# Optimization experiments

Hardware: AMD Instinct MI355X
Metric: run time of the kernel (lower is better)

Reference implementation:

```python
import jax, jax.numpy as jnp
import numpy as np

B, CI, CO, H, W, E, R, K = 32, 128, 256, 64, 64, 8, 16, 3


def setup_inputs() -> dict:
    key = jax.random.key(0)
    ks = jax.random.split(key, 12)
    def n(k, shape, scale):
        return jax.random.normal(k, shape, dtype=jnp.float32) * scale
    return {
        "x": n(ks[0], (B, CI, H, W), 1.0),
        "experts": n(ks[1], (E, CO, CI, K, K), 0.1),
        # routing SE: C -> C/R -> C -> E (1x1 convs == dense on pooled vec)
        "rw1": n(ks[2], (CI // R, CI), 0.05), "rb1": jnp.zeros((CI // R,), jnp.float32),
        "rw2": n(ks[3], (CI, CI // R), 0.05), "rb2": jnp.zeros((CI,), jnp.float32),
        "rw3": n(ks[4], (E, CI), 0.05),      "rb3": jnp.zeros((E,), jnp.float32),
        # channel attention SE on output: CO -> CO/R -> CO
        "aw1": n(ks[5], (CO // R, CO), 0.05), "ab1": jnp.zeros((CO // R,), jnp.float32),
        "aw2": n(ks[6], (CO, CO // R), 0.05), "ab2": jnp.zeros((CO,), jnp.float32),
    }


def reference(x, experts, rw1, rb1, rw2, rb2, rw3, rb3, aw1, ab1, aw2, ab2):
    # --- routing: SE-style gate -> softmax over experts ---
    pooled = x.mean(axis=(2, 3))                       # [B, CI]
    h = jax.nn.relu(pooled @ rw1.T + rb1)              # [B, CI/R]
    s = jax.nn.sigmoid(h @ rw2.T + rb2)                # [B, CI]
    rweights = jax.nn.softmax(s @ rw3.T + rb3, axis=1) # [B, E]
    # --- per-sample expert kernel combination ---
    w = jnp.einsum('be,eoihw->boihw', rweights, experts)  # [B, CO, CI, K, K]
    # --- per-sample conv (== grouped conv with groups=B) via vmap ---
    def conv1(xi, wi):
        # xi: [CI,H,W], wi: [CO,CI,K,K]
        return jax.lax.conv_general_dilated(
            xi[None], wi, window_strides=(1, 1), padding=[(1, 1), (1, 1)],
            dimension_numbers=('NCHW', 'OIHW', 'NCHW'))[0]
    out = jax.vmap(conv1)(x, w)                        # [B, CO, H, W]
    # --- channel attention on output ---
    p = out.mean(axis=(2, 3))                          # [B, CO]
    ca = jax.nn.sigmoid(jax.nn.relu(p @ aw1.T + ab1) @ aw2.T + ab2)
    return out * ca[:, :, None, None]
```

## Files before the change

### kernel.cpp

```cpp
#include <hip/hip_runtime.h>
#include <hip/hip_bf16.h>


#define BB 32
#define CI_ 128
#define CO_ 256
#define HW_ 4096
#define KK 1152

typedef unsigned short u16;
typedef __attribute__((ext_vector_type(8))) __bf16 bf16x8;
typedef __attribute__((ext_vector_type(4))) float floatx4;

typedef const __attribute__((address_space(1))) void* gptr_t;
typedef __attribute__((address_space(3))) void* sptr_t;

__device__ __forceinline__ void gload_lds16(const void* g, void* s) {
  __builtin_amdgcn_global_load_lds((gptr_t)g, (sptr_t)s, 16, 0, 0);
}

__global__ __launch_bounds__(256) void k_stats(const float* __restrict__ x,
                                               float* __restrict__ Sr,
                                               float* __restrict__ pooled,
                                               unsigned* __restrict__ zp) {
  int blk = blockIdx.x;
  if (blk == 0 && threadIdx.x < 64) zp[threadIdx.x] = 0u;
  int b = blk >> 7, ci = blk & 127;
  const float4* xp = (const float4*)(x + ((size_t)(b * CI_ + ci) << 12));
  float T = 0.f, r0 = 0.f, r63 = 0.f, c0 = 0.f, c63 = 0.f;
  __shared__ float corn[4];
  __shared__ float wsum[4][5];
  int tid = threadIdx.x;
  for (int k = 0; k < 4; k++) {
    int i4 = tid + (k << 8);
    float4 v = xp[i4];
    float vv[4] = {v.x, v.y, v.z, v.w};
#pragma unroll
    for (int c = 0; c < 4; c++) {
      int e = (i4 << 2) + c;
      int y = e >> 6, xx = e & 63;
      float val = vv[c];
      T += val;
      if (y == 0) r0 += val;
      if (y == 63) r63 += val;
      if (xx == 0) c0 += val;
      if (xx == 63) c63 += val;
      if (e == 0)    corn[0] = val;
      if (e == 63)   corn[1] = val;
      if (e == 4032) corn[2] = val;
      if (e == 4095) corn[3] = val;
    }
  }
  for (int off = 32; off; off >>= 1) {
    T   += __shfl_down(T, off);
    r0  += __shfl_down(r0, off);
    r63 += __shfl_down(r63, off);
    c0  += __shfl_down(c0, off);
    c63 += __shfl_down(c63, off);
  }
  int w = tid >> 6, lane = tid & 63;
  if (lane == 0) { wsum[w][0]=T; wsum[w][1]=r0; wsum[w][2]=r63; wsum[w][3]=c0; wsum[w][4]=c63; }
  __syncthreads();
  if (tid == 0) {
    T   = wsum[0][0]+wsum[1][0]+wsum[2][0]+wsum[3][0];
    r0  = wsum[0][1]+wsum[1][1]+wsum[2][1]+wsum[3][1];
    r63 = wsum[0][2]+wsum[1][2]+wsum[2][2]+wsum[3][2];
    c0  = wsum[0][3]+wsum[1][3]+wsum[2][3]+wsum[3][3];
    c63 = wsum[0][4]+wsum[1][4]+wsum[2][4]+wsum[3][4];
    pooled[b * CI_ + ci] = T * (1.0f / 4096.0f);
#pragma unroll
    for (int ky = 0; ky < 3; ky++) {
#pragma unroll
      for (int kx = 0; kx < 3; kx++) {
        int dy = ky - 1, dx = kx - 1;
        float s = T;
        if (dy == -1) s -= r63;
        if (dy ==  1) s -= r0;
        if (dx == -1) s -= c63;
        if (dx ==  1) s -= c0;
        if (dy != 0 && dx != 0) s += corn[(dy == -1 ? 2 : 0) + (dx == -1 ? 1 : 0)];
        Sr[(b * 9 + ky * 3 + kx) * CI_ + ci] = s * (1.0f / 4096.0f);
      }
    }
  }
}

__global__ __launch_bounds__(256) void k_transpose(const float* __restrict__ x,
                                                   u16* __restrict__ xt) {
  int blk = blockIdx.x;
  int b = blk >> 6, y = blk & 63;
  __shared__ u16 ts[64][130];
  int tid = threadIdx.x;
  const float* xb = x + ((size_t)b << 19) + (y << 6);
  for (int k = 0; k < 32; k++) {
    int i = tid + (k << 8);
    int ci = i >> 6, xx = i & 63;
    float v = xb[(size_t)ci * 4096 + xx];
    __hip_bfloat16 h = __float2bfloat16(v);
    ts[xx][ci] = *(const u16*)&h;
  }
  __syncthreads();
  uint2* ot = (uint2*)(xt + ((size_t)b * HW_ + y * 64) * CI_);
  for (int k = 0; k < 8; k++) {
    int j = tid + (k << 8);
    int pix = j >> 5, cq = (j & 31) << 2;
    uint2 val;
    u16* pv = (u16*)&val;
    pv[0] = ts[pix][cq]; pv[1] = ts[pix][cq + 1];
    pv[2] = ts[pix][cq + 2]; pv[3] = ts[pix][cq + 3];
    ot[j] = val;
  }
}

__global__ __launch_bounds__(128) void k_route(const float* __restrict__ pooled,
    const float* __restrict__ rw1, const float* __restrict__ rb1,
    const float* __restrict__ rw2, const float* __restrict__ rb2,
    const float* __restrict__ rw3, const float* __restrict__ rb3,
    float* __restrict__ r) {
  int b = blockIdx.x, tid = threadIdx.x;
  __shared__ float ps[128], hs[8], ss[128], lg[8];
  ps[tid] = pooled[b * 128 + tid];
  __syncthreads();
  if (tid < 8) {
    float a = rb1[tid];
    for (int c = 0; c < 128; c++) a += ps[c] * rw1[tid * 128 + c];
    hs[tid] = fmaxf(a, 0.f);
  }
  __syncthreads();
  {
    float a = rb2[tid];
    for (int j = 0; j < 8; j++) a += hs[j] * rw2[tid * 8 + j];
    ss[tid] = 1.f / (1.f + expf(-a));
  }
  __syncthreads();
  if (tid < 8) {
    float a = rb3[tid];
    for (int c = 0; c < 128; c++) a += ss[c] * rw3[tid * 128 + c];
    lg[tid] = a;
  }
  __syncthreads();
  if (tid == 0) {
    float m = lg[0];
    for (int e = 1; e < 8; e++) m = fmaxf(m, lg[e]);
    float s = 0.f, ex[8];
    for (int e = 0; e < 8; e++) { ex[e] = expf(lg[e] - m); s += ex[e]; }
    for (int e = 0; e < 8; e++) r[b * 8 + e] = ex[e] / s;
  }
}

__global__ __launch_bounds__(128) void k_combine(const float* __restrict__ experts,
                                                 const float* __restrict__ r,
                                                 __hip_bfloat16* __restrict__ wr) {
  int blk = blockIdx.x;
  int co = blk >> 5, b = blk & 31;
  int ci = threadIdx.x;
  __shared__ float rs[8];
  if (ci < 8) rs[ci] = r[b * 8 + ci];
  __syncthreads();
  float acc[9] = {0.f, 0.f, 0.f, 0.f, 0.f, 0.f, 0.f, 0.f, 0.f};
  for (int e = 0; e < 8; e++) {
    const float* ep = experts + (((size_t)e * 256 + co) * 128 + ci) * 9;
    float wv = rs[e];
#pragma unroll
    for (int k = 0; k < 9; k++) acc[k] += wv * ep[k];
  }
  __hip_bfloat16* wrow = wr + (size_t)(b * 256 + co) * KK;
#pragma unroll
  for (int k = 0; k < 9; k++) wrow[k * 128 + ci] = __float2bfloat16(acc[k]);
}

__global__ __launch_bounds__(64) void k_pout(const __hip_bfloat16* __restrict__ wr,
                                             const float* __restrict__ Sr,
                                             float* __restrict__ p) {
  int blk = blockIdx.x;
  int b = blk >> 8, co = blk & 255;
  int t = threadIdx.x;
  const __hip_bfloat16* wrow = wr + (size_t)(b * 256 + co) * KK;
  const float* sb = Sr + b * KK;
  float a = 0.f;
  for (int i = t; i < KK; i += 64) a += __bfloat162float(wrow[i]) * sb[i];
  for (int off = 32; off; off >>= 1) a += __shfl_down(a, off);
  if (t == 0) p[b * 256 + co] = a;
}

__global__ __launch_bounds__(256) void k_catt(const float* __restrict__ p,
    const float* __restrict__ aw1, const float* __restrict__ ab1,
    const float* __restrict__ aw2, const float* __restrict__ ab2,
    float* __restrict__ ca) {
  int b = blockIdx.x, tid = threadIdx.x;
  __shared__ float ps[256], ts[16];
  ps[tid] = p[b * 256 + tid];
  __syncthreads();
  if (tid < 16) {
    float a = ab1[tid];
    for (int c = 0; c < 256; c++) a += ps[c] * aw1[tid * 256 + c];
    ts[tid] = fmaxf(a, 0.f);
  }
  __syncthreads();
  float a = ab2[tid];
  for (int j = 0; j < 16; j++) a += ts[j] * aw2[tid * 16 + j];
  ca[b * 256 + tid] = 1.f / (1.f + expf(-a));
}

__global__ __launch_bounds__(256) void k_conv(const u16* __restrict__ xt,
                                              const u16* __restrict__ wr,
                                              const float* __restrict__ ca,
                                              const u16* __restrict__ zp,
                                              float* __restrict__ out) {
  int blk = blockIdx.x;
  int rp = blk & 31, coT = (blk >> 5) & 1, b = blk >> 6;
  int y0 = rp * 2;
  int coBase = coT * 128;
  int tid = threadIdx.x;
  int w = tid >> 6, lane = tid & 63;
  int wm = w & 1, wn = w >> 1;
  int quad = lane >> 4, l15 = lane & 15;
  int cl = lane & 3;

  __shared__ __align__(16) u16 As[128 * 32];
  __shared__ __align__(16) u16 Bs[128 * 32];

  const u16* aSrc[2];
  int dstOff[2], chB[2], ylocB[2], xlocB[2];
#pragma unroll
  for (int inst = 0; inst < 2; inst++) {
    int rr = w * 32 + inst * 16 + (lane >> 2);
    int s = (rr ^ (rr >> 2)) & 3;
    int ch = cl ^ s;
    aSrc[inst] = wr + (size_t)(b * 256 + coBase + rr) * KK + ch * 8;
    dstOff[inst] = (w * 32 + inst * 16) * 32 + lane * 8;
    chB[inst] = ch;
    ylocB[inst] = rr >> 6;
    xlocB[inst] = rr & 63;
  }

  int aOff[4], bOff[4];
#pragma unroll
  for (int i = 0; i < 4; i++) {
    int m = wm * 64 + i * 16 + l15;
    aOff[i] = m * 32 + ((quad ^ ((m ^ (m >> 2)) & 3)) << 3);
    int n = wn * 64 + i * 16 + l15;
    bOff[i] = n * 32 + ((quad ^ ((n ^ (n >> 2)) & 3)) << 3);
  }

  floatx4 acc[4][4];
#pragma unroll
  for (int i = 0; i < 4; i++)
#pragma unroll
    for (int j = 0; j < 4; j++) acc[i][j] = floatx4{0.f, 0.f, 0.f, 0.f};

  for (int kidx = 0; kidx < 9; kidx++) {
    int ky = kidx / 3, kx = kidx - ky * 3;
    const u16* bSrc[2];
#pragma unroll
    for (int inst = 0; inst < 2; inst++) {
      int ys = y0 + ylocB[inst] + ky - 1;
      int xs = xlocB[inst] + kx - 1;
      bool valid = ((unsigned)ys < 64u) && ((unsigned)xs < 64u);
      bSrc[inst] = valid ? (xt + ((size_t)(b * HW_ + ys * 64 + xs) << 7) + chB[inst] * 8)
                         : (zp + chB[inst] * 8);
    }
    const u16* aS0 = aSrc[0] + kidx * 128;
    const u16* aS1 = aSrc[1] + kidx * 128;
#pragma unroll
    for (int cib = 0; cib < 4; cib++) {
      __syncthreads();
      gload_lds16(aS0 + cib * 32, &As[dstOff[0]]);
      gload_lds16(aS1 + cib * 32, &As[dstOff[1]]);
      gload_lds16(bSrc[0] + cib * 32, &Bs[dstOff[0]]);
      gload_lds16(bSrc[1] + cib * 32, &Bs[dstOff[1]]);
      __syncthreads();
      bf16x8 af[4], bfv[4];
#pragma unroll
      for (int i = 0; i < 4; i++) af[i] = *(const bf16x8*)&As[aOff[i]];
#pragma unroll
      for (int j = 0; j < 4; j++) bfv[j] = *(const bf16x8*)&Bs[bOff[j]];
#pragma unroll
      for (int i = 0; i < 4; i++)
#pragma unroll
        for (int j = 0; j < 4; j++)
          acc[i][j] = __builtin_amdgcn_mfma_f32_16x16x32_bf16(af[i], bfv[j], acc[i][j], 0, 0, 0);
    }
  }

  float cav[4][4];
#pragma unroll
  for (int i = 0; i < 4; i++)
#pragma unroll
    for (int ri = 0; ri < 4; ri++)
      cav[i][ri] = ca[b * 256 + coBase + wm * 64 + i * 16 + quad * 4 + ri];
#pragma unroll
  for (int i = 0; i < 4; i++) {
#pragma unroll
    for (int j = 0; j < 4; j++) {
      int n = wn * 64 + j * 16 + l15;
      int yy = y0 + (n >> 6), xx = n & 63;
#pragma unroll
      for (int ri = 0; ri < 4; ri++) {
        int co = coBase + wm * 64 + i * 16 + quad * 4 + ri;
        out[((size_t)(b * 256 + co) << 12) + (yy << 6) + xx] = acc[i][j][ri] * cav[i][ri];
      }
    }
  }
}

extern "C" void kernel_launch(void* const* d_in, const int* in_sizes, int n_in,
                              void* d_out, int out_size, void* d_ws, size_t ws_size,
                              hipStream_t stream) {
  const float* x       = (const float*)d_in[0];
  const float* experts = (const float*)d_in[1];
  const float* rw1 = (const float*)d_in[2];
  const float* rb1 = (const float*)d_in[3];
  const float* rw2 = (const float*)d_in[4];
  const float* rb2 = (const float*)d_in[5];
  const float* rw3 = (const float*)d_in[6];
  const float* rb3 = (const float*)d_in[7];
  const float* aw1 = (const float*)d_in[8];
  const float* ab1 = (const float*)d_in[9];
  const float* aw2 = (const float*)d_in[10];
  const float* ab2 = (const float*)d_in[11];

  char* ws = (char*)d_ws;
  u16*   xt     = (u16*)(ws + 0);
  __hip_bfloat16* wr = (__hip_bfloat16*)(ws + 33554432);
  float* Sr     = (float*)(ws + 52428800);
  float* pooled = (float*)(ws + 52576256);
  float* r      = (float*)(ws + 52592640);
  float* p      = (float*)(ws + 52593664);
  float* ca     = (float*)(ws + 52626432);
  u16*   zp     = (u16*)(ws + 52659200);

  k_stats<<<4096, 256, 0, stream>>>(x, Sr, pooled, (unsigned*)zp);
  k_transpose<<<2048, 256, 0, stream>>>(x, xt);
  k_route<<<32, 128, 0, stream>>>(pooled, rw1, rb1, rw2, rb2, rw3, rb3, r);
  k_combine<<<8192, 128, 0, stream>>>(experts, r, wr);
  k_pout<<<8192, 64, 0, stream>>>(wr, Sr, p);
  k_catt<<<32, 256, 0, stream>>>(p, aw1, ab1, aw2, ab2, ca);
  k_conv<<<2048, 256, 0, stream>>>(xt, (const u16*)wr, ca, zp, (float*)d_out);
}
```

Before: 356.6 us.

## Fuse expert combine with pooled-output dot, vectorize stats/transpose, parallelize SE MLPs

The expert-combine and output-pooling kernels are merged into one kernel per output channel. It stages all eight experts' weights in LDS, reuses them across the whole batch, and computes the pooled-output dot products inline instead of re-reading the combined weights. The stats and transpose kernels now use float4 loads with fewer index branches, and the routing and channel-attention MLPs spread each dot product across 16 lanes with shuffle reductions. The trade-off is that the fused kernel launches only 256 blocks with about 37KB of LDS each, which lowers parallelism and occupancy.

```diff
diff --git a/kernel.cpp b/kernel.cpp
--- a/kernel.cpp
+++ b/kernel.cpp
@@ -19,37 +19,33 @@
   __builtin_amdgcn_global_load_lds((gptr_t)g, (sptr_t)s, 16, 0, 0);
 }
 
-__global__ __launch_bounds__(256) void k_stats(const float* __restrict__ x,
-                                               float* __restrict__ Sr,
-                                               float* __restrict__ pooled,
-                                               unsigned* __restrict__ zp) {
+__global__ __launch_bounds__(256) void k_stats2(const float* __restrict__ x,
+                                                float* __restrict__ Sr,
+                                                float* __restrict__ pooled,
+                                                unsigned* __restrict__ zp) {
   int blk = blockIdx.x;
-  if (blk == 0 && threadIdx.x < 64) zp[threadIdx.x] = 0u;
+  int tid = threadIdx.x;
+  if (blk == 0 && tid < 64) zp[tid] = 0u;
   int b = blk >> 7, ci = blk & 127;
   const float4* xp = (const float4*)(x + ((size_t)(b * CI_ + ci) << 12));
   float T = 0.f, r0 = 0.f, r63 = 0.f, c0 = 0.f, c63 = 0.f;
   __shared__ float corn[4];
   __shared__ float wsum[4][5];
-  int tid = threadIdx.x;
-  for (int k = 0; k < 4; k++) {
-    int i4 = tid + (k << 8);
-    float4 v = xp[i4];
-    float vv[4] = {v.x, v.y, v.z, v.w};
-#pragma unroll
-    for (int c = 0; c < 4; c++) {
-      int e = (i4 << 2) + c;
-      int y = e >> 6, xx = e & 63;
-      float val = vv[c];
-      T += val;
-      if (y == 0) r0 += val;
-      if (y == 63) r63 += val;
-      if (xx == 0) c0 += val;
-      if (xx == 63) c63 += val;
-      if (e == 0)    corn[0] = val;
-      if (e == 63)   corn[1] = val;
-      if (e == 4032) corn[2] = val;
-      if (e == 4095) corn[3] = val;
-    }
+#pragma unroll
+  for (int j = 0; j < 4; j++) {
+    int idx = j * 256 + tid;
+    float4 v = xp[idx];
+    float rs = v.x + v.y + v.z + v.w;
+    T += rs;
+    int x16 = idx & 15;
+    if (idx < 16)    r0  += rs;
+    if (idx >= 1008) r63 += rs;
+    if (x16 == 0)  c0  += v.x;
+    if (x16 == 15) c63 += v.w;
+    if (idx == 0)    corn[0] = v.x;
+    if (idx == 15)   corn[1] = v.w;
+    if (idx == 1008) corn[2] = v.x;
+    if (idx == 1023) corn[3] = v.w;
   }
   for (int off = 32; off; off >>= 1) {
     T   += __shfl_down(T, off);
@@ -85,58 +81,69 @@
   }
 }
 
-__global__ __launch_bounds__(256) void k_transpose(const float* __restrict__ x,
-                                                   u16* __restrict__ xt) {
+__global__ __launch_bounds__(256) void k_xform(const float* __restrict__ x,
+                                               u16* __restrict__ xt) {
   int blk = blockIdx.x;
   int b = blk >> 6, y = blk & 63;
-  __shared__ u16 ts[64][130];
+  __shared__ u16 ts[64][132];
   int tid = threadIdx.x;
   const float* xb = x + ((size_t)b << 19) + (y << 6);
-  for (int k = 0; k < 32; k++) {
-    int i = tid + (k << 8);
-    int ci = i >> 6, xx = i & 63;
-    float v = xb[(size_t)ci * 4096 + xx];
-    __hip_bfloat16 h = __float2bfloat16(v);
-    ts[xx][ci] = *(const u16*)&h;
+#pragma unroll
+  for (int it = 0; it < 8; it++) {
+    int idx = it * 256 + tid;
+    int ci = idx >> 4, x4 = idx & 15;
+    float4 v = *(const float4*)(xb + (size_t)ci * 4096 + x4 * 4);
+    __hip_bfloat16 h0 = __float2bfloat16(v.x), h1 = __float2bfloat16(v.y);
+    __hip_bfloat16 h2 = __float2bfloat16(v.z), h3 = __float2bfloat16(v.w);
+    int xx = x4 << 2;
+    ts[xx + 0][ci] = *(const u16*)&h0;
+    ts[xx + 1][ci] = *(const u16*)&h1;
+    ts[xx + 2][ci] = *(const u16*)&h2;
+    ts[xx + 3][ci] = *(const u16*)&h3;
   }
   __syncthreads();
   uint2* ot = (uint2*)(xt + ((size_t)b * HW_ + y * 64) * CI_);
-  for (int k = 0; k < 8; k++) {
-    int j = tid + (k << 8);
-    int pix = j >> 5, cq = (j & 31) << 2;
-    uint2 val;
-    u16* pv = (u16*)&val;
-    pv[0] = ts[pix][cq]; pv[1] = ts[pix][cq + 1];
-    pv[2] = ts[pix][cq + 2]; pv[3] = ts[pix][cq + 3];
-    ot[j] = val;
-  }
-}
-
-__global__ __launch_bounds__(128) void k_route(const float* __restrict__ pooled,
+#pragma unroll
+  for (int it = 0; it < 8; it++) {
+    int o = it * 256 + tid;
+    int pix = o >> 5, c4 = o & 31;
+    ot[o] = *(const uint2*)&ts[pix][c4 * 4];
+  }
+}
+
+__global__ __launch_bounds__(128) void k_route2(const float* __restrict__ pooled,
     const float* __restrict__ rw1, const float* __restrict__ rb1,
     const float* __restrict__ rw2, const float* __restrict__ rb2,
     const float* __restrict__ rw3, const float* __restrict__ rb3,
     float* __restrict__ r) {
   int b = blockIdx.x, tid = threadIdx.x;
+  int o = tid >> 4, l = tid & 15;
   __shared__ float ps[128], hs[8], ss[128], lg[8];
   ps[tid] = pooled[b * 128 + tid];
   __syncthreads();
-  if (tid < 8) {
-    float a = rb1[tid];
-    for (int c = 0; c < 128; c++) a += ps[c] * rw1[tid * 128 + c];
-    hs[tid] = fmaxf(a, 0.f);
+  {
+    float a = 0.f;
+#pragma unroll
+    for (int j = 0; j < 8; j++) a += ps[l * 8 + j] * rw1[o * 128 + l * 8 + j];
+    a += __shfl_xor(a, 1); a += __shfl_xor(a, 2);
+    a += __shfl_xor(a, 4); a += __shfl_xor(a, 8);
+    if (l == 0) hs[o] = fmaxf(a + rb1[o], 0.f);
   }
   __syncthreads();
   {
     float a = rb2[tid];
+#pragma unroll
     for (int j = 0; j < 8; j++) a += hs[j] * rw2[tid * 8 + j];
     ss[tid] = 1.f / (1.f + expf(-a));
   }
   __syncthreads();
-  if (tid < 8) {
-    float a = rb3[tid];
-    for (int c = 0; c < 128; c++) a += ss[c] * rw3[tid * 128 + c];
-    lg[tid] = a;
+  {
+    float a = 0.f;
+#pragma unroll
+    for (int j = 0; j < 8; j++) a += ss[l * 8 + j] * rw3[o * 128 + l * 8 + j];
+    a += __shfl_xor(a, 1); a += __shfl_xor(a, 2);
+    a += __shfl_xor(a, 4); a += __shfl_xor(a, 8);
+    if (l == 0) lg[o] = a + rb3[o];
   }
   __syncthreads();
   if (tid == 0) {
@@ -148,56 +155,69 @@
   }
 }
 
-__global__ __launch_bounds__(128) void k_combine(const float* __restrict__ experts,
-                                                 const float* __restrict__ r,
-                                                 __hip_bfloat16* __restrict__ wr) {
-  int blk = blockIdx.x;
-  int co = blk >> 5, b = blk & 31;
-  int ci = threadIdx.x;
-  __shared__ float rs[8];
-  if (ci < 8) rs[ci] = r[b * 8 + ci];
-  __syncthreads();
-  float acc[9] = {0.f, 0.f, 0.f, 0.f, 0.f, 0.f, 0.f, 0.f, 0.f};
-  for (int e = 0; e < 8; e++) {
-    const float* ep = experts + (((size_t)e * 256 + co) * 128 + ci) * 9;
-    float wv = rs[e];
-#pragma unroll
-    for (int k = 0; k < 9; k++) acc[k] += wv * ep[k];
-  }
-  __hip_bfloat16* wrow = wr + (size_t)(b * 256 + co) * KK;
-#pragma unroll
-  for (int k = 0; k < 9; k++) wrow[k * 128 + ci] = __float2bfloat16(acc[k]);
-}
-
-__global__ __launch_bounds__(64) void k_pout(const __hip_bfloat16* __restrict__ wr,
-                                             const float* __restrict__ Sr,
-                                             float* __restrict__ p) {
-  int blk = blockIdx.x;
-  int b = blk >> 8, co = blk & 255;
-  int t = threadIdx.x;
-  const __hip_bfloat16* wrow = wr + (size_t)(b * 256 + co) * KK;
-  const float* sb = Sr + b * KK;
-  float a = 0.f;
-  for (int i = t; i < KK; i += 64) a += __bfloat162float(wrow[i]) * sb[i];
-  for (int off = 32; off; off >>= 1) a += __shfl_down(a, off);
-  if (t == 0) p[b * 256 + co] = a;
-}
-
-__global__ __launch_bounds__(256) void k_catt(const float* __restrict__ p,
+__global__ __launch_bounds__(256) void k_combine2(const float* __restrict__ experts,
+                                                  const float* __restrict__ r,
+                                                  const float* __restrict__ Sr,
+                                                  __hip_bfloat16* __restrict__ wr,
+                                                  float* __restrict__ p) {
+  int co = blockIdx.x, tid = threadIdx.x;
+  __shared__ float els[8][1152];
+  __shared__ float rsh[32][8];
+  __shared__ float pw[4];
+#pragma unroll
+  for (int it = 0; it < 9; it++) {
+    int f = it * 256 + tid;
+    int e = f / 288, q = f - e * 288;
+    float4 ev = *(const float4*)(experts + (size_t)e * 294912 + (size_t)co * 1152 + q * 4);
+    *(float4*)&els[e][q * 4] = ev;
+  }
+  rsh[tid >> 3][tid & 7] = r[tid];
+  __syncthreads();
+  int s = tid >> 7, ci = tid & 127;
+  for (int bb = 0; bb < 16; bb++) {
+    int b = bb * 2 + s;
+    float rv[8];
+#pragma unroll
+    for (int e = 0; e < 8; e++) rv[e] = rsh[b][e];
+    float pacc = 0.f;
+    __hip_bfloat16* wrow = wr + (size_t)(b * 256 + co) * KK;
+    const float* sb = Sr + b * KK;
+#pragma unroll
+    for (int k = 0; k < 9; k++) {
+      float v = 0.f;
+#pragma unroll
+      for (int e = 0; e < 8; e++) v += rv[e] * els[e][ci * 9 + k];
+      wrow[k * 128 + ci] = __float2bfloat16(v);
+      pacc += v * sb[k * 128 + ci];
+    }
+    for (int off = 32; off; off >>= 1) pacc += __shfl_down(pacc, off);
+    if ((tid & 63) == 0) pw[tid >> 6] = pacc;
+    __syncthreads();
+    if (ci == 0) p[b * 256 + co] = pw[s * 2] + pw[s * 2 + 1];
+    __syncthreads();
+  }
+}
+
+__global__ __launch_bounds__(256) void k_catt2(const float* __restrict__ p,
     const float* __restrict__ aw1, const float* __restrict__ ab1,
     const float* __restrict__ aw2, const float* __restrict__ ab2,
     float* __restrict__ ca) {
   int b = blockIdx.x, tid = threadIdx.x;
+  int o = tid >> 4, l = tid & 15;
   __shared__ float ps[256], ts[16];
   ps[tid] = p[b * 256 + tid];
   __syncthreads();
-  if (tid < 16) {
-    float a = ab1[tid];
-    for (int c = 0; c < 256; c++) a += ps[c] * aw1[tid * 256 + c];
-    ts[tid] = fmaxf(a, 0.f);
+  {
+    float a = 0.f;
+#pragma unroll
+    for (int j = 0; j < 16; j++) a += ps[l * 16 + j] * aw1[o * 256 + l * 16 + j];
+    a += __shfl_xor(a, 1); a += __shfl_xor(a, 2);
+    a += __shfl_xor(a, 4); a += __shfl_xor(a, 8);
+    if (l == 0) ts[o] = fmaxf(a + ab1[o], 0.f);
   }
   __syncthreads();
   float a = ab2[tid];
+#pragma unroll
   for (int j = 0; j < 16; j++) a += ts[j] * aw2[tid * 16 + j];
   ca[b * 256 + tid] = 1.f / (1.f + expf(-a));
 }
@@ -330,11 +350,10 @@
   float* ca     = (float*)(ws + 52626432);
   u16*   zp     = (u16*)(ws + 52659200);
 
-  k_stats<<<4096, 256, 0, stream>>>(x, Sr, pooled, (unsigned*)zp);
-  k_transpose<<<2048, 256, 0, stream>>>(x, xt);
-  k_route<<<32, 128, 0, stream>>>(pooled, rw1, rb1, rw2, rb2, rw3, rb3, r);
-  k_combine<<<8192, 128, 0, stream>>>(experts, r, wr);
-  k_pout<<<8192, 64, 0, stream>>>(wr, Sr, p);
-  k_catt<<<32, 256, 0, stream>>>(p, aw1, ab1, aw2, ab2, ca);
+  k_stats2<<<4096, 256, 0, stream>>>(x, Sr, pooled, (unsigned*)zp);
+  k_xform<<<2048, 256, 0, stream>>>(x, xt);
+  k_route2<<<32, 128, 0, stream>>>(pooled, rw1, rb1, rw2, rb2, rw3, rb3, r);
+  k_combine2<<<256, 256, 0, stream>>>(experts, r, Sr, wr, p);
+  k_catt2<<<32, 256, 0, stream>>>(p, aw1, ab1, aw2, ab2, ca);
   k_conv<<<2048, 256, 0, stream>>>(xt, (const u16*)wr, ca, zp, (float*)d_out);
 }
```

Measured after the change: 332.5 us. -6.8%, faster.
